# Kernel optimization log

Measured on AMD Instinct MI355X. Metric: run time of the kernel, lower is better.

The kernel has to match this reference:

```python
import jax, jax.numpy as jnp
import numpy as np

NEG_SLOPE = 0.01  # nn.LeakyReLU default

def _lrelu(v):
    return jnp.where(v >= 0, v, NEG_SLOPE * v)

def setup_inputs() -> dict:
    key = jax.random.key(0)
    ks = jax.random.split(key, 12)
    B, C, T = 16, 512, 128
    s = 0.02
    d = {
        'out1': jax.random.normal(ks[0], (B, C, T), jnp.float32),
        'out2': jax.random.normal(ks[1], (B, C, T), jnp.float32),
        'out3': jax.random.normal(ks[2], (B, C, T), jnp.float32),
        'theta_w': jax.random.normal(ks[3], (C, C), jnp.float32) * s,
        'phi_w':   jax.random.normal(ks[4], (C, C), jnp.float32) * s,
        'g_w':     jax.random.normal(ks[5], (C, C), jnp.float32) * s,
        'W_w':     jax.random.normal(ks[6], (C, C), jnp.float32) * s,
        'W_b':     jax.random.normal(ks[7], (C,),  jnp.float32) * s,
        'p1_w':    jax.random.normal(ks[8], (C, C), jnp.float32) * s,
        'p2_w':    jax.random.normal(ks[9], (C, C), jnp.float32) * s,
        'p3_w':    jax.random.normal(ks[10], (1, C), jnp.float32) * s,
        'p3_b':    jax.random.normal(ks[11], (1,),  jnp.float32) * s,
        'window_size': 8,
    }
    return d

def reference(out1, out2, out3, theta_w, phi_w, g_w, W_w, W_b,
              p1_w, p2_w, p3_w, p3_b, window_size):
    B, C, T = out1.shape
    w = window_size
    # stack three encoder streams: [B, C, T, 3]
    x = jnp.stack([out1, out2, out3], axis=3)
    # left-pad time axis with zeros (new_out[:, :, w-1:, :] = out)
    padded = jnp.pad(x, ((0, 0), (0, 0), (w - 1, 0), (0, 0)))
    # sliding windows over all T timesteps at once: [B, C, T, w, 3]
    idx = jnp.arange(T)[:, None] + jnp.arange(w)[None, :]
    win = padded[:, :, idx, :]
    N = w * 3  # tokens per window
    X = win.transpose(0, 2, 1, 3, 4).reshape(B, T, C, N)  # [B,T,C,N]
    # embedded-Gaussian non-local block (1x1 convs == channel matmuls)
    theta = jnp.einsum('oc,btcn->bton', theta_w, X)
    phi   = jnp.einsum('oc,btcn->bton', phi_w, X)
    g     = jnp.einsum('oc,btcn->bton', g_w, X)
    f = jnp.einsum('bton,btom->btnm', theta, phi)   # theta^T phi
    f_div = jax.nn.softmax(f, axis=-1)
    y = jnp.einsum('btnm,btom->bton', f_div, g)
    W_y = jnp.einsum('oc,btcn->bton', W_w, y) + W_b[None, None, :, None]
    z = W_y + X                                       # residual
    # AdaptiveMaxPool2d((1,1)) over the window tokens -> [B,T,C]
    pooled = jnp.max(z, axis=-1)
    h = pooled.transpose(1, 0, 2)                     # [T,B,C]
    # projector MLP (dropout = identity at inference)
    h = _lrelu(h @ p1_w.T)
    h = _lrelu(h @ p2_w.T)
    out = _lrelu(h @ p3_w.T + p3_b)                   # [T,B,1]
    return out
```

## Files before the change

### kernel.cpp

```cpp
#include <hip/hip_runtime.h>

typedef __attribute__((ext_vector_type(8))) short short8;
typedef __attribute__((ext_vector_type(4))) float float4v;
typedef __attribute__((ext_vector_type(4))) unsigned int uint4v;
typedef __attribute__((ext_vector_type(4))) unsigned short ushort4v;

__device__ __forceinline__ float lrelu(float v) { return v >= 0.f ? v : 0.01f * v; }

__device__ __forceinline__ unsigned short f2bf(float x) {
    union { float f; unsigned u; } c; c.f = x;
    unsigned r = (c.u + 0x7FFFu + ((c.u >> 16) & 1u)) >> 16;
    return (unsigned short)r;
}
__device__ __forceinline__ float bf2f(unsigned short h) {
    union { unsigned u; float f; } c; c.u = ((unsigned)h) << 16;
    return c.f;
}

__device__ __forceinline__ void gload16(const unsigned short* g, unsigned short* l) {
    __builtin_amdgcn_global_load_lds(
        (const __attribute__((address_space(1))) unsigned int*)g,
        (__attribute__((address_space(3))) unsigned int*)l, 16, 0, 0);
}

__device__ __forceinline__ void mfma_core(
    const unsigned short* __restrict__ Ah, const unsigned short* __restrict__ Al, int lda,
    const unsigned short* __restrict__ Bh, const unsigned short* __restrict__ Bl, int ldb,
    unsigned short* lds, float4v acc[4][4]) {
    const int tid = threadIdx.x;
    const int lane = tid & 63, wave = tid >> 6;
    const int wm = wave >> 1, wn = wave & 1;
    const int l15 = lane & 15, lhi = lane >> 4;
    unsigned short* LAh = lds;
    unsigned short* LAl = lds + 8192;
    unsigned short* LBh = lds + 16384;
    unsigned short* LBl = lds + 24576;

    for (int k0 = 0; k0 < 512; k0 += 64) {
#pragma unroll
        for (int tile = 0; tile < 4; ++tile) {
            const unsigned short* s = (tile == 0) ? Ah : (tile == 1) ? Al : (tile == 2) ? Bh : Bl;
            int ld = (tile < 2) ? lda : ldb;
            unsigned short* dbase = lds + tile * 8192;
#pragma unroll
            for (int it = 0; it < 4; ++it) {
                int idx = it * 256 + tid;
                int row = idx >> 3, ch = idx & 7;
                gload16(&s[row * ld + k0 + ((ch ^ (row & 7)) << 3)],
                        dbase + ((it * 256 + wave * 64) << 3));
            }
        }
        __syncthreads();
#pragma unroll
        for (int ks = 0; ks < 2; ++ks) {
            short8 ah[4], al[4], bh[4], bl[4];
#pragma unroll
            for (int m = 0; m < 4; ++m) {
                int r = wm * 64 + m * 16 + l15;
                int off = r * 64 + (((ks * 4 + lhi) ^ (r & 7)) * 8);
                ah[m] = *(const short8*)&LAh[off];
                al[m] = *(const short8*)&LAl[off];
            }
#pragma unroll
            for (int n = 0; n < 4; ++n) {
                int r = wn * 64 + n * 16 + l15;
                int off = r * 64 + (((ks * 4 + lhi) ^ (r & 7)) * 8);
                bh[n] = *(const short8*)&LBh[off];
                bl[n] = *(const short8*)&LBl[off];
            }
#pragma unroll
            for (int m = 0; m < 4; ++m)
#pragma unroll
                for (int n = 0; n < 4; ++n) {
                    acc[m][n] = __builtin_amdgcn_mfma_f32_16x16x32_bf16(ah[m], bh[n], acc[m][n], 0, 0, 0);
                    acc[m][n] = __builtin_amdgcn_mfma_f32_16x16x32_bf16(ah[m], bl[n], acc[m][n], 0, 0, 0);
                    acc[m][n] = __builtin_amdgcn_mfma_f32_16x16x32_bf16(al[m], bh[n], acc[m][n], 0, 0, 0);
                }
        }
        __syncthreads();
    }
}

__global__ __launch_bounds__(256) void k_splitw6(
    const float* __restrict__ tw, const float* __restrict__ fw,
    const float* __restrict__ gw, const float* __restrict__ ww,
    const float* __restrict__ p1w, const float* __restrict__ p2w,
    unsigned short* __restrict__ TtH, unsigned short* __restrict__ TtL,
    unsigned short* __restrict__ PtH, unsigned short* __restrict__ PtL,
    unsigned short* __restrict__ GtH, unsigned short* __restrict__ GtL,
    unsigned short* __restrict__ WwH, unsigned short* __restrict__ WwL,
    unsigned short* __restrict__ p1h, unsigned short* __restrict__ p1l,
    unsigned short* __restrict__ p2h, unsigned short* __restrict__ p2l) {
    int z = blockIdx.z;
    int i0 = blockIdx.x * 32, k0 = blockIdx.y * 32;
    int tx = threadIdx.x, ty = threadIdx.y;
    __shared__ float tile[32][33];
    if (z < 3) {
        const float* src = (z == 0) ? tw : (z == 1) ? fw : gw;
        unsigned short* dh = (z == 0) ? TtH : (z == 1) ? PtH : GtH;
        unsigned short* dl = (z == 0) ? TtL : (z == 1) ? PtL : GtL;
#pragma unroll
        for (int i = 0; i < 4; ++i)
            tile[ty + i * 8][tx] = src[(k0 + ty + i * 8) * 512 + i0 + tx];
        __syncthreads();
#pragma unroll
        for (int i = 0; i < 4; ++i) {
            int row = i0 + ty + i * 8;
            float v = tile[tx][ty + i * 8];
            unsigned short h = f2bf(v), l = f2bf(v - bf2f(h));
            int idx = row * 512 + k0 + tx;
            dh[idx] = h;
            dl[idx] = l;
        }
    } else {
        const float* src = (z == 3) ? ww : (z == 4) ? p1w : p2w;
        unsigned short* dh = (z == 3) ? WwH : (z == 4) ? p1h : p2h;
        unsigned short* dl = (z == 3) ? WwL : (z == 4) ? p1l : p2l;
#pragma unroll
        for (int i = 0; i < 4; ++i) {
            int r = k0 + ty + i * 8;
            int idx = r * 512 + i0 + tx;
            float v = src[idx];
            unsigned short h = f2bf(v), l = f2bf(v - bf2f(h));
            dh[idx] = h;
            dl[idx] = l;
        }
    }
}

__global__ __launch_bounds__(256) void k_wgemm(
    const unsigned short* __restrict__ WwH, const unsigned short* __restrict__ WwL,
    const unsigned short* __restrict__ GtH, const unsigned short* __restrict__ GtL,
    const unsigned short* __restrict__ TtH, const unsigned short* __restrict__ TtL,
    const unsigned short* __restrict__ PtH, const unsigned short* __restrict__ PtL,
    unsigned short* __restrict__ Whi, unsigned short* __restrict__ Wlo) {
    __shared__ unsigned short lds[32768];
    int i0 = blockIdx.y * 128, j0 = blockIdx.x * 128;
    bool wg = blockIdx.z == 0;
    const unsigned short* Ah = (wg ? WwH : TtH) + i0 * 512;
    const unsigned short* Al = (wg ? WwL : TtL) + i0 * 512;
    const unsigned short* Bh = (wg ? GtH : PtH) + j0 * 512;
    const unsigned short* Bl = (wg ? GtL : PtL) + j0 * 512;
    float4v acc[4][4];
#pragma unroll
    for (int m = 0; m < 4; ++m)
#pragma unroll
        for (int n = 0; n < 4; ++n) acc[m][n] = (float4v){0.f, 0.f, 0.f, 0.f};

    mfma_core(Ah, Al, 512, Bh, Bl, 512, lds, acc);

    int lane = threadIdx.x & 63, wave = threadIdx.x >> 6;
    int wm = wave >> 1, wn = wave & 1, l15 = lane & 15, lhi = lane >> 4;
    int rowbase = wg ? 512 + i0 : i0;
#pragma unroll
    for (int m = 0; m < 4; ++m)
#pragma unroll
        for (int n = 0; n < 4; ++n) {
            int bcol = j0 + wn * 64 + n * 16 + l15;
#pragma unroll
            for (int i = 0; i < 4; ++i) {
                int r = rowbase + wm * 64 + m * 16 + lhi * 4 + i;
                float v = acc[m][n][i];
                unsigned short h = f2bf(v), l = f2bf(v - bf2f(h));
                Whi[r * 512 + bcol] = h;
                Wlo[r * 512 + bcol] = l;
            }
        }
}

__global__ __launch_bounds__(256) void k_splitx(const float* __restrict__ o1,
                                                const float* __restrict__ o2,
                                                const float* __restrict__ o3,
                                                unsigned short* __restrict__ Xh,
                                                unsigned short* __restrict__ Xl,
                                                float* __restrict__ Xf) {
    int z = blockIdx.z;
    int b = z / 3, k = z - b * 3;
    const float* In = (k == 0) ? o1 : ((k == 1) ? o2 : o3);
    int c0 = blockIdx.x * 32, t0 = blockIdx.y * 32;
    __shared__ float tile[32][33];
    int tx = threadIdx.x, ty = threadIdx.y;
#pragma unroll
    for (int i = 0; i < 4; ++i)
        tile[ty + i * 8][tx] = In[(b * 512 + c0 + ty + i * 8) * 128 + t0 + tx];
    __syncthreads();
#pragma unroll
    for (int i = 0; i < 4; ++i) {
        int t = t0 + ty + i * 8;
        float v = tile[tx][ty + i * 8];
        unsigned short h = f2bf(v), l = f2bf(v - bf2f(h));
        int idx = ((b * 128 + t) * 3 + k) * 512 + c0 + tx;
        Xh[idx] = h;
        Xl[idx] = l;
        Xf[idx] = v;
    }
}

__global__ __launch_bounds__(256) void k_ga(
    const unsigned short* __restrict__ Whi, const unsigned short* __restrict__ Wlo,
    const unsigned short* __restrict__ Xh, const unsigned short* __restrict__ Xl,
    unsigned short* __restrict__ Yh, unsigned short* __restrict__ Yl,
    float* __restrict__ Wg) {
    __shared__ unsigned short lds[32768];
    int bk = blockIdx.x, y = blockIdx.y;
    int b = bk / 3, kin = bk - b * 3;
    int bbase = (b * 384 + kin) * 512;
    float4v acc[4][4];
#pragma unroll
    for (int m = 0; m < 4; ++m)
#pragma unroll
        for (int n = 0; n < 4; ++n) acc[m][n] = (float4v){0.f, 0.f, 0.f, 0.f};

    mfma_core(Whi + y * 128 * 512, Wlo + y * 128 * 512, 512,
              Xh + bbase, Xl + bbase, 1536, lds, acc);

    int lane = threadIdx.x & 63, wave = threadIdx.x >> 6;
    int wm = wave >> 1, wn = wave & 1, l15 = lane & 15, lhi = lane >> 4;
    int wsel = y >> 2, o0 = (y & 3) * 128;
#pragma unroll
    for (int m = 0; m < 4; ++m)
#pragma unroll
        for (int n = 0; n < 4; ++n) {
            int o_in = wm * 64 + m * 16 + lhi * 4;
            int t = wn * 64 + n * 16 + l15;
            int idx = bbase + t * 1536 + o0 + o_in;
            if (wsel == 1) {
                *(float4v*)&Wg[idx] = acc[m][n];
            } else {
                ushort4v h, l;
#pragma unroll
                for (int i = 0; i < 4; ++i) {
                    float v = acc[m][n][i];
                    h[i] = f2bf(v);
                    l[i] = f2bf(v - bf2f(h[i]));
                }
                *(ushort4v*)&Yh[idx] = h;
                *(ushort4v*)&Yl[idx] = l;
            }
        }
}

__global__ __launch_bounds__(64) void k_gram3(
    const unsigned short* __restrict__ Xh, const unsigned short* __restrict__ Xl,
    const unsigned short* __restrict__ Yh, const unsigned short* __restrict__ Yl,
    float* __restrict__ D) {
    __shared__ unsigned short lds[8192];
    int orig = blockIdx.x;
    int idx = (orig & 7) * 144 + (orig >> 3);
    int mat = idx >> 3, c = idx & 7;
    int b = mat / 9, r9 = mat - b * 9, k = r9 / 3, kp = r9 - k * 3;
    const unsigned short* Ahg = Xh + (b * 384 + k) * 512;
    const unsigned short* Alg = Xl + (b * 384 + k) * 512;
    const unsigned short* Bhg = Yh + (b * 384 + kp) * 512;
    const unsigned short* Blg = Yl + (b * 384 + kp) * 512;
    int t1b = c * 16, t2b0 = c * 16 - 16;
    unsigned short* LAh = lds;
    unsigned short* LAl = lds + 1024;
    unsigned short* LBh = lds + 2048;
    unsigned short* LBl = lds + 5120;
    int tid = threadIdx.x;
    int l15 = tid & 15, lhi = tid >> 4;
    float4v acc[3];
    acc[0] = (float4v){0.f, 0.f, 0.f, 0.f};
    acc[1] = (float4v){0.f, 0.f, 0.f, 0.f};
    acc[2] = (float4v){0.f, 0.f, 0.f, 0.f};

    for (int k0 = 0; k0 < 512; k0 += 64) {
#pragma unroll
        for (int it = 0; it < 2; ++it) {
            int i2 = it * 64 + tid;
            int row = i2 >> 3, ch = i2 & 7;
            int g = (t1b + row) * 1536 + k0 + ((ch ^ (row & 7)) << 3);
            gload16(&Ahg[g], LAh + ((it * 64) << 3));
            gload16(&Alg[g], LAl + ((it * 64) << 3));
        }
#pragma unroll
        for (int it = 0; it < 6; ++it) {
            int i2 = it * 64 + tid;
            int row = i2 >> 3, ch = i2 & 7;
            int t2 = t2b0 + row;
            int t2c = t2 < 0 ? 0 : (t2 > 127 ? 127 : t2);
            int g = t2c * 1536 + k0 + ((ch ^ (row & 7)) << 3);
            gload16(&Bhg[g], LBh + ((it * 64) << 3));
            gload16(&Blg[g], LBl + ((it * 64) << 3));
        }
        __syncthreads();
#pragma unroll
        for (int ks = 0; ks < 2; ++ks) {
            int offa = l15 * 64 + (((ks * 4 + lhi) ^ (l15 & 7)) * 8);
            short8 ah = *(const short8*)&LAh[offa];
            short8 al = *(const short8*)&LAl[offa];
#pragma unroll
            for (int tl = 0; tl < 3; ++tl) {
                int rb = tl * 16 + l15;
                int offb = rb * 64 + (((ks * 4 + lhi) ^ (rb & 7)) * 8);
                short8 bh = *(const short8*)&LBh[offb];
                short8 bl = *(const short8*)&LBl[offb];
                acc[tl] = __builtin_amdgcn_mfma_f32_16x16x32_bf16(ah, bh, acc[tl], 0, 0, 0);
                acc[tl] = __builtin_amdgcn_mfma_f32_16x16x32_bf16(ah, bl, acc[tl], 0, 0, 0);
                acc[tl] = __builtin_amdgcn_mfma_f32_16x16x32_bf16(al, bh, acc[tl], 0, 0, 0);
            }
        }
        __syncthreads();
    }
    float* Dm = D + mat * 16384;
#pragma unroll
    for (int tl = 0; tl < 3; ++tl) {
        int t2base = t2b0 + tl * 16;
        if (t2base < 0 || t2base > 127) continue;
        int t2 = t2base + l15;
#pragma unroll
        for (int i = 0; i < 4; ++i) {
            int t1 = t1b + lhi * 4 + i;
            Dm[t1 * 128 + t2] = acc[tl][i];
        }
    }
}

template <bool SPLIT_OUT>
__global__ __launch_bounds__(256) void k_mlp(
    const unsigned short* __restrict__ Ahi, const unsigned short* __restrict__ Alo,
    const unsigned short* __restrict__ Bhi, const unsigned short* __restrict__ Blo,
    unsigned short* __restrict__ Ch, unsigned short* __restrict__ Cl,
    float* __restrict__ Cf) {
    __shared__ unsigned short lds[32768];
    int r0 = blockIdx.x * 128, o0 = blockIdx.y * 128;
    float4v acc[4][4];
#pragma unroll
    for (int m = 0; m < 4; ++m)
#pragma unroll
        for (int n = 0; n < 4; ++n) acc[m][n] = (float4v){0.f, 0.f, 0.f, 0.f};

    mfma_core(Ahi + r0 * 512, Alo + r0 * 512, 512, Bhi + o0 * 512, Blo + o0 * 512, 512, lds, acc);

    int lane = threadIdx.x & 63, wave = threadIdx.x >> 6;
    int wm = wave >> 1, wn = wave & 1, l15 = lane & 15, lhi = lane >> 4;
#pragma unroll
    for (int m = 0; m < 4; ++m)
#pragma unroll
        for (int n = 0; n < 4; ++n) {
            int o = o0 + wn * 64 + n * 16 + l15;
#pragma unroll
            for (int i = 0; i < 4; ++i) {
                int r = r0 + wm * 64 + m * 16 + lhi * 4 + i;
                float v = lrelu(acc[m][n][i]);
                if (SPLIT_OUT) {
                    unsigned short h = f2bf(v), l = f2bf(v - bf2f(h));
                    Ch[r * 512 + o] = h;
                    Cl[r * 512 + o] = l;
                } else {
                    Cf[r * 512 + o] = v;
                }
            }
        }
}

__global__ __launch_bounds__(512) void k_mix(
    const float* __restrict__ Xf, const float* __restrict__ Wg,
    const float* __restrict__ D, const float* __restrict__ W_b,
    unsigned short* __restrict__ Plh, unsigned short* __restrict__ Pll) {
    int orig = blockIdx.x;
    int bid = ((orig & 7) << 6) | (orig >> 3);
    int b = bid >> 5, tg = bid & 31;
    int t0 = tg * 4;
    int tid = threadIdx.x;

    __shared__ float Pm[4][24][28];

    for (int idx = tid; idx < 4 * 576; idx += 512) {
        int dt = idx / 576, r = idx - dt * 576;
        int n = r / 24, m = r - n * 24;
        int t = t0 + dt;
        int j = n / 3, k = n - j * 3;
        int jp = m / 3, kp = m - jp * 3;
        int t1 = t - 7 + j, t2 = t - 7 + jp;
        float v = 0.f;
        if (t1 >= 0 && t2 >= 0)
            v = D[((((b * 3 + k) * 3 + kp) * 128 + t1) << 7) + t2];
        Pm[dt][n][m] = v;
    }
    __syncthreads();

    if (tid < 96) {
        int dt = tid / 24, n = tid - dt * 24;
        float mx = -1e30f;
#pragma unroll
        for (int m = 0; m < 24; ++m) mx = fmaxf(mx, Pm[dt][n][m]);
        float e[24], sum = 0.f;
#pragma unroll
        for (int m = 0; m < 24; ++m) { e[m] = __expf(Pm[dt][n][m] - mx); sum += e[m]; }
        float inv = 1.0f / sum;
#pragma unroll
        for (int m = 0; m < 24; ++m) Pm[dt][n][m] = e[m] * inv;
    }
    __syncthreads();

    int o = tid;
    float wg[33], xw[33];
#pragma unroll
    for (int s = 0; s < 11; ++s) {
        int tp = t0 - 7 + s;
#pragma unroll
        for (int k = 0; k < 3; ++k) {
            int base = (((b * 128 + tp) * 3 + k) << 9) + o;
            bool ok = (tp >= 0);
            wg[s * 3 + k] = ok ? Wg[base] : 0.f;
            xw[s * 3 + k] = ok ? Xf[base] : 0.f;
        }
    }
    float wb = W_b[o];
#pragma unroll
    for (int dt = 0; dt < 4; ++dt) {
        float pooled = -1e30f;
#pragma unroll
        for (int n = 0; n < 24; ++n) {
            float s0 = 0.f, s1 = 0.f, s2 = 0.f, s3 = 0.f;
#pragma unroll
            for (int mq = 0; mq < 6; ++mq) {
                float4 p4 = *(const float4*)&Pm[dt][n][mq * 4];
                s0 += p4.x * wg[mq * 4 + 0 + dt * 3];
                s1 += p4.y * wg[mq * 4 + 1 + dt * 3];
                s2 += p4.z * wg[mq * 4 + 2 + dt * 3];
                s3 += p4.w * wg[mq * 4 + 3 + dt * 3];
            }
            float s = ((s0 + s1) + (s2 + s3)) + wb + xw[n + dt * 3];
            pooled = fmaxf(pooled, s);
        }
        int t = t0 + dt;
        int oidx = ((t * 16 + b) << 9) + o;
        unsigned short h = f2bf(pooled), l = f2bf(pooled - bf2f(h));
        Plh[oidx] = h;
        Pll[oidx] = l;
    }
}

__global__ __launch_bounds__(256) void k_final(const float* __restrict__ H,
                                               const float* __restrict__ p3w,
                                               const float* __restrict__ p3b,
                                               float* __restrict__ out) {
    int r = blockIdx.x * 4 + (threadIdx.x >> 6);
    int lane = threadIdx.x & 63;
    const float4* h4 = (const float4*)&H[r << 9];
    const float4* w4 = (const float4*)p3w;
    float4 a1 = h4[lane], a2 = h4[lane + 64];
    float4 b1 = w4[lane], b2 = w4[lane + 64];
    float s = a1.x * b1.x + a1.y * b1.y + a1.z * b1.z + a1.w * b1.w +
              a2.x * b2.x + a2.y * b2.y + a2.z * b2.z + a2.w * b2.w;
#pragma unroll
    for (int off = 32; off; off >>= 1) s += __shfl_down(s, off, 64);
    if (lane == 0) out[r] = lrelu(s + p3b[0]);
}

extern "C" void kernel_launch(void* const* d_in, const int* in_sizes, int n_in,
                              void* d_out, int out_size, void* d_ws, size_t ws_size,
                              hipStream_t stream) {
    const float* out1 = (const float*)d_in[0];
    const float* out2 = (const float*)d_in[1];
    const float* out3 = (const float*)d_in[2];
    const float* theta_w = (const float*)d_in[3];
    const float* phi_w = (const float*)d_in[4];
    const float* g_w = (const float*)d_in[5];
    const float* W_w = (const float*)d_in[6];
    const float* W_b = (const float*)d_in[7];
    const float* p1_w = (const float*)d_in[8];
    const float* p2_w = (const float*)d_in[9];
    const float* p3_w = (const float*)d_in[10];
    const float* p3_b = (const float*)d_in[11];
    float* outp = (float*)d_out;

    char* wsb = (char*)d_ws;
    unsigned short* Whi = (unsigned short*)(wsb + 0);
    unsigned short* Wlo = (unsigned short*)(wsb + 1048576);
    unsigned short* p1h = (unsigned short*)(wsb + 2097152);
    unsigned short* p1l = (unsigned short*)(wsb + 2621440);
    unsigned short* p2h = (unsigned short*)(wsb + 3145728);
    unsigned short* p2l = (unsigned short*)(wsb + 3670016);
    unsigned short* WwH = (unsigned short*)(wsb + 4194304);
    unsigned short* WwL = (unsigned short*)(wsb + 4718592);
    unsigned short* TtH = (unsigned short*)(wsb + 5242880);
    unsigned short* TtL = (unsigned short*)(wsb + 5767168);
    unsigned short* PtH = (unsigned short*)(wsb + 6291456);
    unsigned short* PtL = (unsigned short*)(wsb + 6815744);
    unsigned short* GtH = (unsigned short*)(wsb + 7340032);
    unsigned short* GtL = (unsigned short*)(wsb + 7864320);
    unsigned short* Xh  = (unsigned short*)(wsb + 8388608);
    unsigned short* Xl  = (unsigned short*)(wsb + 14680064);
    unsigned short* Yh  = (unsigned short*)(wsb + 20971520);
    unsigned short* Yl  = (unsigned short*)(wsb + 27262976);
    float* Wg = (float*)(wsb + 33554432);
    float* D  = (float*)(wsb + 46137344);
    float* Xf = (float*)(wsb + 55574528);
    unsigned short* Plh = (unsigned short*)(wsb + 20971520);
    unsigned short* Pll = (unsigned short*)(wsb + 23068672);
    unsigned short* h1h = (unsigned short*)(wsb + 27262976);
    unsigned short* h1l = (unsigned short*)(wsb + 29360128);
    float* h2 = (float*)(wsb + 8388608);

    k_splitw6<<<dim3(16, 16, 6), dim3(32, 8), 0, stream>>>(
        theta_w, phi_w, g_w, W_w, p1_w, p2_w,
        TtH, TtL, PtH, PtL, GtH, GtL, WwH, WwL, p1h, p1l, p2h, p2l);
    k_splitx<<<dim3(16, 4, 48), dim3(32, 8), 0, stream>>>(out1, out2, out3, Xh, Xl, Xf);
    k_wgemm<<<dim3(4, 4, 2), 256, 0, stream>>>(WwH, WwL, GtH, GtL, TtH, TtL,
                                               PtH, PtL, Whi, Wlo);
    k_ga<<<dim3(48, 8), 256, 0, stream>>>(Whi, Wlo, Xh, Xl, Yh, Yl, Wg);
    k_gram3<<<dim3(1152), 64, 0, stream>>>(Xh, Xl, Yh, Yl, D);
    k_mix<<<dim3(512), 512, 0, stream>>>(Xf, Wg, D, W_b, Plh, Pll);
    k_mlp<true><<<dim3(16, 4), 256, 0, stream>>>(Plh, Pll, p1h, p1l, h1h, h1l, nullptr);
    k_mlp<false><<<dim3(16, 4), 256, 0, stream>>>(h1h, h1l, p2h, p2l, nullptr, nullptr, h2);
    k_final<<<dim3(512), 256, 0, stream>>>(h2, p3_w, p3_b, outp);
}
```

Before: 134.1 us.

## Split-K the weight-product and MLP GEMMs with separate reduction kernels

The small weight-combination GEMM (32 blocks) and the two projector MLP GEMMs (64 blocks each) are split along K into 4 and 2 slices, so more workgroups run on the many CUs. Each slice writes fp32 partials to scratch, reusing the Wg/D workspace regions. A new reduction kernel then sums the partials and applies LeakyReLU and the bf16 hi/lo split where needed. This adds three extra launches and extra global traffic for the partials in exchange for better CU occupancy on undersized grids.

Result: faster. 122.9 us (-8.4%).

```diff
diff --git a/kernel.cpp b/kernel.cpp
--- a/kernel.cpp
+++ b/kernel.cpp
@@ -26,7 +26,7 @@
 __device__ __forceinline__ void mfma_core(
     const unsigned short* __restrict__ Ah, const unsigned short* __restrict__ Al, int lda,
     const unsigned short* __restrict__ Bh, const unsigned short* __restrict__ Bl, int ldb,
-    unsigned short* lds, float4v acc[4][4]) {
+    unsigned short* lds, float4v acc[4][4], int kBeg, int kEnd) {
     const int tid = threadIdx.x;
     const int lane = tid & 63, wave = tid >> 6;
     const int wm = wave >> 1, wn = wave & 1;
@@ -36,7 +36,7 @@
     unsigned short* LBh = lds + 16384;
     unsigned short* LBl = lds + 24576;
 
-    for (int k0 = 0; k0 < 512; k0 += 64) {
+    for (int k0 = kBeg; k0 < kEnd; k0 += 64) {
 #pragma unroll
         for (int tile = 0; tile < 4; ++tile) {
             const unsigned short* s = (tile == 0) ? Ah : (tile == 1) ? Al : (tile == 2) ? Bh : Bl;
@@ -128,30 +128,31 @@
     }
 }
 
-__global__ __launch_bounds__(256) void k_wgemm(
+__global__ __launch_bounds__(256) void k_wgemm_sk(
     const unsigned short* __restrict__ WwH, const unsigned short* __restrict__ WwL,
     const unsigned short* __restrict__ GtH, const unsigned short* __restrict__ GtL,
     const unsigned short* __restrict__ TtH, const unsigned short* __restrict__ TtL,
     const unsigned short* __restrict__ PtH, const unsigned short* __restrict__ PtL,
-    unsigned short* __restrict__ Whi, unsigned short* __restrict__ Wlo) {
+    float* __restrict__ Pw) {
     __shared__ unsigned short lds[32768];
     int i0 = blockIdx.y * 128, j0 = blockIdx.x * 128;
-    bool wg = blockIdx.z == 0;
-    const unsigned short* Ah = (wg ? WwH : TtH) + i0 * 512;
-    const unsigned short* Al = (wg ? WwL : TtL) + i0 * 512;
-    const unsigned short* Bh = (wg ? GtH : PtH) + j0 * 512;
-    const unsigned short* Bl = (wg ? GtL : PtL) + j0 * 512;
+    int wg = blockIdx.z >> 2, kslice = blockIdx.z & 3;
+    const unsigned short* Ah = (wg == 0 ? WwH : TtH) + i0 * 512;
+    const unsigned short* Al = (wg == 0 ? WwL : TtL) + i0 * 512;
+    const unsigned short* Bh = (wg == 0 ? GtH : PtH) + j0 * 512;
+    const unsigned short* Bl = (wg == 0 ? GtL : PtL) + j0 * 512;
     float4v acc[4][4];
 #pragma unroll
     for (int m = 0; m < 4; ++m)
 #pragma unroll
         for (int n = 0; n < 4; ++n) acc[m][n] = (float4v){0.f, 0.f, 0.f, 0.f};
 
-    mfma_core(Ah, Al, 512, Bh, Bl, 512, lds, acc);
+    mfma_core(Ah, Al, 512, Bh, Bl, 512, lds, acc, kslice * 128, kslice * 128 + 128);
 
     int lane = threadIdx.x & 63, wave = threadIdx.x >> 6;
     int wm = wave >> 1, wn = wave & 1, l15 = lane & 15, lhi = lane >> 4;
-    int rowbase = wg ? 512 + i0 : i0;
+    int rowbase = (wg == 0) ? 512 + i0 : i0;
+    float* P = Pw + kslice * 524288;
 #pragma unroll
     for (int m = 0; m < 4; ++m)
 #pragma unroll
@@ -160,12 +161,40 @@
 #pragma unroll
             for (int i = 0; i < 4; ++i) {
                 int r = rowbase + wm * 64 + m * 16 + lhi * 4 + i;
-                float v = acc[m][n][i];
-                unsigned short h = f2bf(v), l = f2bf(v - bf2f(h));
-                Whi[r * 512 + bcol] = h;
-                Wlo[r * 512 + bcol] = l;
-            }
-        }
+                P[r * 512 + bcol] = acc[m][n][i];
+            }
+        }
+}
+
+template <int NPART, int MODE>
+__global__ __launch_bounds__(256) void k_red(
+    const float* __restrict__ P, int stride,
+    unsigned short* __restrict__ Ch, unsigned short* __restrict__ Cl,
+    float* __restrict__ Cf) {
+    int i4 = blockIdx.x * 256 + threadIdx.x;
+    float4v v = ((const float4v*)P)[i4];
+#pragma unroll
+    for (int p = 1; p < NPART; ++p) {
+        float4v u = ((const float4v*)(P + (size_t)p * stride))[i4];
+#pragma unroll
+        for (int j = 0; j < 4; ++j) v[j] += u[j];
+    }
+    if (MODE >= 1) {
+#pragma unroll
+        for (int j = 0; j < 4; ++j) v[j] = lrelu(v[j]);
+    }
+    if (MODE == 2) {
+        ((float4v*)Cf)[i4] = v;
+    } else {
+        ushort4v h, l;
+#pragma unroll
+        for (int j = 0; j < 4; ++j) {
+            h[j] = f2bf(v[j]);
+            l[j] = f2bf(v[j] - bf2f(h[j]));
+        }
+        ((ushort4v*)Ch)[i4] = h;
+        ((ushort4v*)Cl)[i4] = l;
+    }
 }
 
 __global__ __launch_bounds__(256) void k_splitx(const float* __restrict__ o1,
@@ -212,7 +241,7 @@
         for (int n = 0; n < 4; ++n) acc[m][n] = (float4v){0.f, 0.f, 0.f, 0.f};
 
     mfma_core(Whi + y * 128 * 512, Wlo + y * 128 * 512, 512,
-              Xh + bbase, Xl + bbase, 1536, lds, acc);
+              Xh + bbase, Xl + bbase, 1536, lds, acc, 0, 512);
 
     int lane = threadIdx.x & 63, wave = threadIdx.x >> 6;
     int wm = wave >> 1, wn = wave & 1, l15 = lane & 15, lhi = lane >> 4;
@@ -317,24 +346,25 @@
     }
 }
 
-template <bool SPLIT_OUT>
-__global__ __launch_bounds__(256) void k_mlp(
+__global__ __launch_bounds__(256) void k_mlp_sk(
     const unsigned short* __restrict__ Ahi, const unsigned short* __restrict__ Alo,
     const unsigned short* __restrict__ Bhi, const unsigned short* __restrict__ Blo,
-    unsigned short* __restrict__ Ch, unsigned short* __restrict__ Cl,
-    float* __restrict__ Cf) {
+    float* __restrict__ Pp) {
     __shared__ unsigned short lds[32768];
     int r0 = blockIdx.x * 128, o0 = blockIdx.y * 128;
+    int kslice = blockIdx.z;
     float4v acc[4][4];
 #pragma unroll
     for (int m = 0; m < 4; ++m)
 #pragma unroll
         for (int n = 0; n < 4; ++n) acc[m][n] = (float4v){0.f, 0.f, 0.f, 0.f};
 
-    mfma_core(Ahi + r0 * 512, Alo + r0 * 512, 512, Bhi + o0 * 512, Blo + o0 * 512, 512, lds, acc);
+    mfma_core(Ahi + r0 * 512, Alo + r0 * 512, 512, Bhi + o0 * 512, Blo + o0 * 512, 512,
+              lds, acc, kslice * 256, kslice * 256 + 256);
 
     int lane = threadIdx.x & 63, wave = threadIdx.x >> 6;
     int wm = wave >> 1, wn = wave & 1, l15 = lane & 15, lhi = lane >> 4;
+    float* P = Pp + (size_t)kslice * 1048576;
 #pragma unroll
     for (int m = 0; m < 4; ++m)
 #pragma unroll
@@ -343,14 +373,7 @@
 #pragma unroll
             for (int i = 0; i < 4; ++i) {
                 int r = r0 + wm * 64 + m * 16 + lhi * 4 + i;
-                float v = lrelu(acc[m][n][i]);
-                if (SPLIT_OUT) {
-                    unsigned short h = f2bf(v), l = f2bf(v - bf2f(h));
-                    Ch[r * 512 + o] = h;
-                    Cl[r * 512 + o] = l;
-                } else {
-                    Cf[r * 512 + o] = v;
-                }
+                P[r * 512 + o] = acc[m][n][i];
             }
         }
 }
@@ -490,6 +513,8 @@
     float* Wg = (float*)(wsb + 33554432);
     float* D  = (float*)(wsb + 46137344);
     float* Xf = (float*)(wsb + 55574528);
+    float* Pw = Wg;
+    float* Pp = D;
     unsigned short* Plh = (unsigned short*)(wsb + 20971520);
     unsigned short* Pll = (unsigned short*)(wsb + 23068672);
     unsigned short* h1h = (unsigned short*)(wsb + 27262976);
@@ -500,12 +525,15 @@
         theta_w, phi_w, g_w, W_w, p1_w, p2_w,
         TtH, TtL, PtH, PtL, GtH, GtL, WwH, WwL, p1h, p1l, p2h, p2l);
     k_splitx<<<dim3(16, 4, 48), dim3(32, 8), 0, stream>>>(out1, out2, out3, Xh, Xl, Xf);
-    k_wgemm<<<dim3(4, 4, 2), 256, 0, stream>>>(WwH, WwL, GtH, GtL, TtH, TtL,
-                                               PtH, PtL, Whi, Wlo);
+    k_wgemm_sk<<<dim3(4, 4, 8), 256, 0, stream>>>(WwH, WwL, GtH, GtL, TtH, TtL,
+                                                  PtH, PtL, Pw);
+    k_red<4, 0><<<dim3(512), 256, 0, stream>>>(Pw, 524288, Whi, Wlo, nullptr);
     k_ga<<<dim3(48, 8), 256, 0, stream>>>(Whi, Wlo, Xh, Xl, Yh, Yl, Wg);
     k_gram3<<<dim3(1152), 64, 0, stream>>>(Xh, Xl, Yh, Yl, D);
     k_mix<<<dim3(512), 512, 0, stream>>>(Xf, Wg, D, W_b, Plh, Pll);
-    k_mlp<true><<<dim3(16, 4), 256, 0, stream>>>(Plh, Pll, p1h, p1l, h1h, h1l, nullptr);
-    k_mlp<false><<<dim3(16, 4), 256, 0, stream>>>(h1h, h1l, p2h, p2l, nullptr, nullptr, h2);
+    k_mlp_sk<<<dim3(16, 4, 2), 256, 0, stream>>>(Plh, Pll, p1h, p1l, Pp);
+    k_red<2, 1><<<dim3(1024), 256, 0, stream>>>(Pp, 1048576, h1h, h1l, nullptr);
+    k_mlp_sk<<<dim3(16, 4, 2), 256, 0, stream>>>(h1h, h1l, p2h, p2l, Pp);
+    k_red<2, 2><<<dim3(1024), 256, 0, stream>>>(Pp, 1048576, nullptr, nullptr, h2);
     k_final<<<dim3(512), 256, 0, stream>>>(h2, p3_w, p3_b, outp);
 }
```
